# Kernel optimization log

Measured on AMD Instinct MI355X. Metric: run time of the kernel, lower is better.

Reference implementation:

```python
import jax, jax.numpy as jnp
import numpy as np

B, N, K = 4, 16384, 8
NF = [8, 32, 64, 128, 256]
E = N * K


def setup_inputs() -> dict:
    key = jax.random.key(0)
    ks = jax.random.split(key, 16)
    x = jax.random.normal(ks[0], (B, N, NF[0]), jnp.float32)
    # knn-style edge list: every node appears as a center K times (no empty segments)
    centers = jnp.tile(jnp.repeat(jnp.arange(N), K)[None, None, :], (B, 1, 1))
    neighbors = jax.random.randint(ks[1], (B, 1, E), 0, N)
    edge_index = jnp.concatenate([centers, neighbors], axis=1)
    specs = [("0a", NF[0], NF[1]), ("0b", NF[0], NF[1]),
             ("1a", NF[1], NF[2]), ("1b", NF[1], NF[2]),
             ("2a", NF[2], NF[3]), ("2b", NF[2], NF[3]),
             ("3a", NF[3], NF[4]), ("3b", NF[3], NF[4]),
             ("cat", NF[1] + NF[2] + NF[3] + NF[4], 1)]
    inp = {"x": x, "edge_index": edge_index}
    for i, (nm, ci, co) in enumerate(specs):
        inp["W" + nm] = jax.random.normal(ks[2 + i], (ci, co), jnp.float32) / np.sqrt(ci)
        inp["g" + nm] = jnp.ones((co,), jnp.float32)   # BN gamma
        inp["b" + nm] = jnp.zeros((co,), jnp.float32)  # BN beta
    inp["bias"] = jnp.zeros((1,), jnp.float32)
    return inp


def _bn(x, g, b):
    # training-mode BatchNorm1d over all rows (GraphBatchNorm1d reduces over batch*num_points)
    m = x.mean(0)
    v = jnp.mean(jnp.square(x - m), 0)  # biased variance, as torch BN uses for normalization
    return g * (x - m) * jax.lax.rsqrt(v + 1e-5) + b


def _mlp(x, W, g, b):
    # Linear(bias=False) -> BN -> LeakyReLU(0.2)
    return jax.nn.leaky_relu(_bn(x @ W, g, b), negative_slope=0.2)


def reference(x, edge_index,
              W0a, g0a, b0a, W0b, g0b, b0b,
              W1a, g1a, b1a, W1b, g1b, b1b,
              W2a, g2a, b2a, W2b, g2b, b2b,
              W3a, g3a, b3a, W3b, g3b, b3b,
              Wcat, gcat, bcat, bias):
    BN = B * N
    xf = x.reshape(BN, NF[0])
    ei = edge_index.transpose(1, 0, 2).reshape(2, -1)  # [2, B*E]
    off = jnp.repeat(jnp.arange(B) * N, E)
    centers = ei[0] + off
    neighbors = ei[1] + off
    segmax = lambda v: jax.ops.segment_max(v, centers, num_segments=BN)
    x0 = _mlp(xf, W0a, g0a, b0a) + segmax(_mlp(xf[neighbors] - xf[centers], W0b, g0b, b0b))
    x1 = _mlp(x0, W1a, g1a, b1a) + segmax(_mlp(x0, W1b, g1b, b1b)[neighbors])
    x2 = _mlp(x1, W2a, g2a, b2a) + segmax(_mlp(x1, W2b, g2b, b2b)[neighbors])
    x3 = _mlp(x2, W3a, g3a, b3a) + segmax(_mlp(x2, W3b, g3b, b3b)[neighbors])
    x_cat = _mlp(jnp.concatenate([x0, x1, x2, x3], axis=-1), Wcat, gcat, bcat)
    return x_cat + bias
```

## Files before the change

### kernel.cpp

```cpp
#include <hip/hip_runtime.h>
#include <math.h>

static constexpr int BB = 4;
static constexpr int NN = 16384;
static constexpr int KK = 8;
static constexpr int EE = 131072;
static constexpr int RR = 65536;
static constexpr int EG = 524288;

static constexpr int SPL = 64;
static constexpr size_t SLOT = (size_t)SPL*512;

static constexpr size_t OFF_X0 = 0;
static constexpr size_t OFF_X1 = OFF_X0 + (size_t)RR*32;
static constexpr size_t OFF_X2 = OFF_X1 + (size_t)RR*64;
static constexpr size_t OFF_X3 = OFF_X2 + (size_t)RR*128;
static constexpr size_t OFF_ZB = OFF_X3 + (size_t)RR*256;
static constexpr size_t OFF_ZC = OFF_ZB + (size_t)RR*128;
static constexpr size_t OFF_S  = OFF_ZC + (size_t)RR;
static constexpr size_t OFF_WP = OFF_S + 9*SLOT;
static constexpr size_t WP1_OFF = 0;
static constexpr size_t WP2_OFF = 4096;
static constexpr size_t WP3_OFF = 4096 + 16384;

__device__ __forceinline__ float lrelu(float x) { return fmaxf(x, 0.2f*x); }

__device__ __forceinline__ unsigned short f2h(float f) {
    _Float16 h = (_Float16)f;
    return *(unsigned short*)&h;
}
__device__ __forceinline__ float h2f(unsigned short u) {
    _Float16 h = *(_Float16*)&u;
    return (float)h;
}

typedef __attribute__((ext_vector_type(8))) _Float16 half8v;
typedef __attribute__((ext_vector_type(8))) unsigned short ushort8v;
typedef __attribute__((ext_vector_type(4))) float float4v;

__global__ __launch_bounds__(256) void k_l0_node(const float* __restrict__ xf,
                                                 const float* __restrict__ W,
                                                 unsigned short* __restrict__ z,
                                                 float* __restrict__ S) {
    __shared__ float w[256];
    __shared__ float red[64];
    int tid = threadIdx.x;
    w[tid] = W[tid];
    if (tid < 64) red[tid] = 0.f;
    __syncthreads();
    int r = blockIdx.x*256 + tid;
    const float4* xr = (const float4*)(xf + (size_t)r*8);
    float4 a = xr[0], b = xr[1];
    float xv[8] = {a.x,a.y,a.z,a.w,b.x,b.y,b.z,b.w};
    float op[32];
#pragma unroll
    for (int c = 0; c < 32; ++c) {
        float s = 0.f;
#pragma unroll
        for (int k = 0; k < 8; ++k) s = fmaf(xv[k], w[k*32+c], s);
        op[c] = s;
    }
    ushort8v* zp = (ushort8v*)(z + (size_t)r*32);
#pragma unroll
    for (int i = 0; i < 4; ++i) {
        ushort8v h;
#pragma unroll
        for (int j = 0; j < 8; ++j) h[j] = f2h(op[i*8+j]);
        zp[i] = h;
    }
#pragma unroll
    for (int c = 0; c < 32; ++c) {
        float s = op[c], q = op[c]*op[c];
#pragma unroll
        for (int off = 32; off >= 1; off >>= 1) {
            s += __shfl_xor(s, off, 64);
            q += __shfl_xor(q, off, 64);
        }
        if ((tid & 63) == 0) { atomicAdd(&red[c], s); atomicAdd(&red[32+c], q); }
    }
    __syncthreads();
    if (tid < 64) atomicAdd(&S[(size_t)(blockIdx.x & (SPL-1))*512 + tid], red[tid]);
}

__global__ __launch_bounds__(256) void k_edge_stats(const float* __restrict__ xf,
                                                    const int* __restrict__ ei,
                                                    const float* __restrict__ W,
                                                    float* __restrict__ S) {
    __shared__ float w[256];
    __shared__ float red[64];
    int tid = threadIdx.x;
    w[tid] = W[tid];
    if (tid < 64) red[tid] = 0.f;
    __syncthreads();
    int g = tid & 3;
    int cg = g*8;
    float s[8], q[8];
#pragma unroll
    for (int j = 0; j < 8; ++j) { s[j] = 0.f; q[j] = 0.f; }
    int qid = (blockIdx.x*256 + tid) >> 2;
    int NQ = (gridDim.x*256) >> 2;
    for (int e = qid; e < EG; e += NQ) {
        int b = e >> 17, jj = e & (EE-1);
        const int* base = ei + (size_t)b*2*EE;
        int ctr = base[jj], nbr = base[EE + jj];
        const float4* pc = (const float4*)(xf + ((size_t)(b<<14) + ctr)*8);
        const float4* pn = (const float4*)(xf + ((size_t)(b<<14) + nbr)*8);
        float4 c0 = pc[0], c1 = pc[1], n0 = pn[0], n1 = pn[1];
        float d[8] = {n0.x-c0.x, n0.y-c0.y, n0.z-c0.z, n0.w-c0.w,
                      n1.x-c1.x, n1.y-c1.y, n1.z-c1.z, n1.w-c1.w};
#pragma unroll
        for (int j = 0; j < 8; ++j) {
            int c = cg + j;
            float z = 0.f;
#pragma unroll
            for (int k = 0; k < 8; ++k) z = fmaf(d[k], w[k*32+c], z);
            s[j] += z; q[j] = fmaf(z, z, q[j]);
        }
    }
#pragma unroll
    for (int off = 4; off <= 32; off <<= 1) {
#pragma unroll
        for (int j = 0; j < 8; ++j) {
            s[j] += __shfl_xor(s[j], off, 64);
            q[j] += __shfl_xor(q[j], off, 64);
        }
    }
    if ((tid & 63) < 4) {
#pragma unroll
        for (int j = 0; j < 8; ++j) {
            atomicAdd(&red[cg + j], s[j]);
            atomicAdd(&red[32 + cg + j], q[j]);
        }
    }
    __syncthreads();
    if (tid < 64) atomicAdd(&S[(size_t)(blockIdx.x & (SPL-1))*512 + tid], red[tid]);
}

__global__ __launch_bounds__(256) void k_edge_apply(const float* __restrict__ xf,
                                                    const int* __restrict__ ei,
                                                    const float* __restrict__ W,
                                                    const float* __restrict__ Sa,
                                                    const float* __restrict__ Sb,
                                                    const float* __restrict__ ga,
                                                    const float* __restrict__ ba,
                                                    const float* __restrict__ gb,
                                                    const float* __restrict__ bbp,
                                                    const float* __restrict__ Wc,
                                                    unsigned short* __restrict__ x0,
                                                    float* __restrict__ zc) {
    __shared__ float w[256];
    __shared__ float scb[32], shb[32], sca[32], sha[32], swc[32];
    int tid = threadIdx.x;
    w[tid] = W[tid];
    if (tid < 32) {
        float su = 0.f, qu = 0.f;
        for (int p = 0; p < SPL; ++p) { su += Sa[(size_t)p*512 + tid]; qu += Sa[(size_t)p*512 + 32 + tid]; }
        float m = su*(1.f/RR);
        float v = fmaxf(qu*(1.f/RR) - m*m, 0.f);
        float sc = ga[tid]*rsqrtf(v + 1e-5f);
        sca[tid] = sc; sha[tid] = fmaf(-m, sc, ba[tid]);
        swc[tid] = Wc[tid];
    } else if (tid < 64) {
        int c = tid - 32;
        float su = 0.f, qu = 0.f;
        for (int p = 0; p < SPL; ++p) { su += Sb[(size_t)p*512 + c]; qu += Sb[(size_t)p*512 + 32 + c]; }
        float m = su*(1.f/EG);
        float v = fmaxf(qu*(1.f/EG) - m*m, 0.f);
        float sc = gb[c]*rsqrtf(v + 1e-5f);
        scb[c] = sc; shb[c] = fmaf(-m, sc, bbp[c]);
    }
    __syncthreads();
    int r = blockIdx.x*256 + tid;
    int b = r >> 14, n = r & (NN-1);
    const int* nb = ei + (size_t)b*2*EE + EE + n*KK;
    const float4* pc = (const float4*)(xf + (size_t)r*8);
    float4 c0 = pc[0], c1 = pc[1];
    float mx[32];
#pragma unroll
    for (int c = 0; c < 32; ++c) mx[c] = -3.0e38f;
    for (int k = 0; k < KK; ++k) {
        int j = nb[k];
        const float4* pn = (const float4*)(xf + ((size_t)(b<<14) + j)*8);
        float4 n0 = pn[0], n1 = pn[1];
        float d[8] = {n0.x-c0.x, n0.y-c0.y, n0.z-c0.z, n0.w-c0.w,
                      n1.x-c1.x, n1.y-c1.y, n1.z-c1.z, n1.w-c1.w};
#pragma unroll
        for (int c = 0; c < 32; ++c) {
            float z = 0.f;
#pragma unroll
            for (int k2 = 0; k2 < 8; ++k2) z = fmaf(d[k2], w[k2*32+c], z);
            float y = lrelu(fmaf(z, scb[c], shb[c]));
            mx[c] = fmaxf(mx[c], y);
        }
    }
    ushort8v* xp = (ushort8v*)(x0 + (size_t)r*32);
    float sdot = 0.f;
#pragma unroll
    for (int i = 0; i < 4; ++i) {
        ushort8v v = xp[i];
        ushort8v o;
#pragma unroll
        for (int j = 0; j < 8; ++j) {
            int c = i*8 + j;
            float val = lrelu(fmaf(h2f(v[j]), sca[c], sha[c])) + mx[c];
            o[j] = f2h(val);
            sdot = fmaf(val, swc[c], sdot);
        }
        xp[i] = o;
    }
    zc[r] = sdot;
}

template<int CI, int CO>
__global__ __launch_bounds__(256) void k_packW(const float* __restrict__ Wa,
                                               const float* __restrict__ Wb,
                                               unsigned short* __restrict__ Wp) {
    constexpr int NT = 2*CO;
    constexpr int KT = CI/32;
    int t = blockIdx.x*256 + threadIdx.x;
    if (t >= NT*CI) return;
    int ng = t % NT, k = t / NT;
    float v = (ng < CO) ? Wa[(size_t)k*CO + ng] : Wb[(size_t)k*CO + (ng - CO)];
    int nt = ng >> 4, n = ng & 15;
    int kt = k >> 5, kq = (k & 31) >> 3, j = k & 7;
    int f = nt*KT + kt;
    int idx = f*512 + ((kq*16 + n)<<3) + j;
    Wp[idx] = f2h(v);
}

template<int CI, int CO, int NCH, int MR>
__global__ __launch_bounds__(256, 4) void k_mfma_dual(const unsigned short* __restrict__ X,
                                                      const unsigned short* __restrict__ Wp,
                                                      unsigned short* __restrict__ Za,
                                                      unsigned short* __restrict__ Zb,
                                                      float* __restrict__ Sa,
                                                      float* __restrict__ Sb) {
    constexpr int KT = CI/32;
    constexpr int WCNT = NCH*KT*512;
    constexpr int ROWT = RR/(MR*16);
    constexpr int STR = NCH*16 + 8;
    constexpr int XW  = (CI < 64) ? CI : 64;
    constexpr int PLB = CO/64;
    __shared__ unsigned short Wlds[WCNT];
    __shared__ unsigned short scr[4][16*STR];
    int tid = threadIdx.x;
    int lane = tid & 63, wid = tid >> 6;
    int ch = blockIdx.y;
    int wglob = blockIdx.x*4 + wid;
    int NW = gridDim.x*4;
    int n = lane & 15, kq = lane >> 4;
    int rg = lane >> 3, c8l = (lane & 7)*8;
    unsigned short* myscr = scr[wid];
    size_t pl = (size_t)(wglob & (SPL-1)) * 512;
    bool isA = (ch < PLB);
    unsigned short* Zp = (isA ? Za : Zb) + (size_t)(isA ? ch : ch - PLB)*((size_t)RR*64);
    {
        const ushort8v* src = (const ushort8v*)(Wp + (size_t)ch*WCNT);
        ushort8v* dst = (ushort8v*)Wlds;
        for (int u = tid; u < WCNT/8; u += 256) dst[u] = src[u];
    }
    __syncthreads();

    for (int t = wglob; t < ROWT; t += NW) {
        size_t rowbase = (size_t)t * (MR*16);
        float4v acc[MR][NCH];
#pragma unroll
        for (int i = 0; i < MR; ++i)
#pragma unroll
            for (int j = 0; j < NCH; ++j)
                acc[i][j] = (float4v){0.f, 0.f, 0.f, 0.f};
#pragma unroll
        for (int kt = 0; kt < KT; ++kt) {
            int k0 = kt*32 + kq*8;
            int xpl = k0 >> 6;
            int xoff = k0 & (XW-1);
            const unsigned short* Xp = X + (size_t)xpl*((size_t)RR*64);
            half8v b[MR];
#pragma unroll
            for (int i = 0; i < MR; ++i)
                b[i] = *(const half8v*)&Xp[(rowbase + i*16 + n)*XW + xoff];
#pragma unroll
            for (int j = 0; j < NCH; ++j) {
                half8v w = *(const half8v*)&Wlds[(j*KT + kt)*512 + lane*8];
#pragma unroll
                for (int i = 0; i < MR; ++i)
                    acc[i][j] = __builtin_amdgcn_mfma_f32_16x16x32_f16(w, b[i], acc[i][j], 0, 0, 0);
            }
        }
#pragma unroll
        for (int j = 0; j < NCH; ++j) {
            int colg = ch*64 + j*16;
            float* Sg = isA ? Sa : Sb;
            int cb = isA ? colg : colg - CO;
#pragma unroll
            for (int reg = 0; reg < 4; ++reg) {
                float s = 0.f, q = 0.f;
#pragma unroll
                for (int i = 0; i < MR; ++i) {
                    float v = acc[i][j][reg];
                    s += v; q = fmaf(v, v, q);
                }
                s += __shfl_xor(s, 1, 64); q += __shfl_xor(q, 1, 64);
                s += __shfl_xor(s, 2, 64); q += __shfl_xor(q, 2, 64);
                s += __shfl_xor(s, 4, 64); q += __shfl_xor(q, 4, 64);
                s += __shfl_xor(s, 8, 64); q += __shfl_xor(q, 8, 64);
                if (n == 0) {
                    int col = cb + kq*4 + reg;
                    atomicAdd(&Sg[pl + col], s);
                    atomicAdd(&Sg[pl + CO + col], q);
                }
            }
        }
#pragma unroll
        for (int i = 0; i < MR; ++i) {
            __builtin_amdgcn_wave_barrier();
#pragma unroll
            for (int j = 0; j < NCH; ++j) {
                float4v a4 = acc[i][j];
                ushort4 h = { f2h(a4[0]), f2h(a4[1]), f2h(a4[2]), f2h(a4[3]) };
                *(ushort4*)&myscr[n*STR + j*16 + kq*4] = h;
            }
            __builtin_amdgcn_wave_barrier();
#pragma unroll
            for (int i2 = 0; i2 < 2; ++i2) {
                int rit = rg + i2*8;
                ushort8v v = *(const ushort8v*)&myscr[rit*STR + c8l];
                *(ushort8v*)&Zp[(rowbase + i*16 + rit)*64 + c8l] = v;
            }
        }
    }
}

template<int CO>
__global__ __launch_bounds__(256) void k_redstats(float* __restrict__ Sa,
                                                  float* __restrict__ Sb) {
    int t = blockIdx.x*256 + threadIdx.x;
    for (int u = t; u < 2*CO; u += gridDim.x*256) {
        float sa = 0.f, sb = 0.f;
        for (int p = 1; p < SPL; ++p) {
            sa += Sa[(size_t)p*512 + u];
            sb += Sb[(size_t)p*512 + u];
        }
        Sa[u] += sa;
        Sb[u] += sb;
    }
}

template<int CO, bool WRITEBACK>
__global__ __launch_bounds__(256) void k_gathermax(unsigned short* __restrict__ xi,
                                                   const unsigned short* __restrict__ zbh,
                                                   const int* __restrict__ ei,
                                                   const float* __restrict__ Sa,
                                                   const float* __restrict__ Sb,
                                                   const float* __restrict__ ga,
                                                   const float* __restrict__ ba,
                                                   const float* __restrict__ gb,
                                                   const float* __restrict__ bbp,
                                                   const float* __restrict__ Wc,
                                                   int wcoff,
                                                   float* __restrict__ zc) {
    constexpr int CQ = CO/8;
    __shared__ float sca[CO], sha[CO], scb[CO], shb[CO], swc[CO];
    int tid = threadIdx.x;
    for (int u = tid; u < CO; u += 256) {
        float m = Sa[u]*(1.f/RR);
        float v = fmaxf(Sa[CO+u]*(1.f/RR) - m*m, 0.f);
        float sc = ga[u]*rsqrtf(v + 1e-5f);
        sca[u] = sc; sha[u] = fmaf(-m, sc, ba[u]);
        m = Sb[u]*(1.f/RR);
        v = fmaxf(Sb[CO+u]*(1.f/RR) - m*m, 0.f);
        sc = gb[u]*rsqrtf(v + 1e-5f);
        scb[u] = sc; shb[u] = fmaf(-m, sc, bbp[u]);
        swc[u] = Wc[wcoff + u];
    }
    __syncthreads();
    int t = blockIdx.x*256 + tid;
    int r = t / CQ;
    int c8 = (t % CQ)*8;
    int pln = c8 >> 6;
    int off = c8 & 63;
    const unsigned short* zpl = zbh + (size_t)pln*((size_t)RR*64);
    unsigned short* xpl = xi + (size_t)pln*((size_t)RR*64);
    int b = r >> 14, n = r & (NN-1);
    const int* nb = ei + (size_t)b*2*EE + EE + n*KK;
    float sb[8], hb[8];
#pragma unroll
    for (int j = 0; j < 8; ++j) { sb[j] = scb[c8+j]; hb[j] = shb[c8+j]; }
    int nbr[KK];
#pragma unroll
    for (int k = 0; k < KK; ++k) nbr[k] = nb[k];
    size_t bb64 = ((size_t)(b<<14))*64 + off;
    float mx[8];
#pragma unroll
    for (int j = 0; j < 8; ++j) mx[j] = -3e38f;
#pragma unroll
    for (int k = 0; k < KK; ++k) {
        ushort8v u = *(const ushort8v*)(zpl + bb64 + (size_t)nbr[k]*64);
#pragma unroll
        for (int j = 0; j < 8; ++j)
            mx[j] = fmaxf(mx[j], lrelu(fmaf(h2f(u[j]), sb[j], hb[j])));
    }
    ushort8v* xp = (ushort8v*)&xpl[(size_t)r*64 + off];
    ushort8v a = *xp;
    float sdot = 0.f;
    if (WRITEBACK) {
        ushort8v o;
#pragma unroll
        for (int j = 0; j < 8; ++j) {
            float val = lrelu(fmaf(h2f(a[j]), sca[c8+j], sha[c8+j])) + mx[j];
            o[j] = f2h(val);
            sdot = fmaf(val, swc[c8+j], sdot);
        }
        *xp = o;
    } else {
#pragma unroll
        for (int j = 0; j < 8; ++j) {
            float val = lrelu(fmaf(h2f(a[j]), sca[c8+j], sha[c8+j])) + mx[j];
            sdot = fmaf(val, swc[c8+j], sdot);
        }
    }
#pragma unroll
    for (int w = CQ/2; w >= 1; w >>= 1) sdot += __shfl_xor(sdot, w, 64);
    int lane = tid & 63;
    if ((lane & (CQ-1)) == 0) atomicAdd(&zc[r], sdot);
}

__global__ __launch_bounds__(256) void k_catstats(const float* __restrict__ zc,
                                                  float* __restrict__ S8) {
    __shared__ float rs2[2];
    int tid = threadIdx.x;
    if (tid < 2) rs2[tid] = 0.f;
    __syncthreads();
    float v = zc[blockIdx.x*256 + tid];
    float s = v, q = v*v;
#pragma unroll
    for (int off = 32; off >= 1; off >>= 1) {
        s += __shfl_xor(s, off, 64);
        q += __shfl_xor(q, off, 64);
    }
    if ((tid & 63) == 0) { atomicAdd(&rs2[0], s); atomicAdd(&rs2[1], q); }
    __syncthreads();
    if (tid == 0) {
        int p = blockIdx.x & 255;
        atomicAdd(&S8[p*2],     rs2[0]);
        atomicAdd(&S8[p*2 + 1], rs2[1]);
    }
}

__global__ __launch_bounds__(256) void k_catfinal(const float* __restrict__ zc,
                                                  const float* __restrict__ S8,
                                                  const float* __restrict__ g,
                                                  const float* __restrict__ bb,
                                                  const float* __restrict__ bias,
                                                  float* __restrict__ out) {
    __shared__ float rs[256], rq[256];
    int tid = threadIdx.x;
    rs[tid] = S8[tid*2];
    rq[tid] = S8[tid*2 + 1];
    __syncthreads();
#pragma unroll
    for (int h = 128; h >= 1; h >>= 1) {
        if (tid < h) { rs[tid] += rs[tid+h]; rq[tid] += rq[tid+h]; }
        __syncthreads();
    }
    int r = blockIdx.x*256 + tid;
    const float invR = 1.f/65536.f;
    float m = rs[0]*invR;
    float v = fmaxf(rq[0]*invR - m*m, 0.f);
    float sc = g[0]*rsqrtf(v + 1e-5f);
    float sh = fmaf(-m, sc, bb[0]);
    float y = lrelu(fmaf(zc[r], sc, sh));
    out[r] = y + bias[0];
}

extern "C" void kernel_launch(void* const* d_in, const int* in_sizes, int n_in,
                              void* d_out, int out_size, void* d_ws, size_t ws_size,
                              hipStream_t stream) {
    const float* x    = (const float*)d_in[0];
    const int*   ei   = (const int*)d_in[1];
    const float* W0a  = (const float*)d_in[2];
    const float* g0a  = (const float*)d_in[3];
    const float* b0a  = (const float*)d_in[4];
    const float* W0b  = (const float*)d_in[5];
    const float* g0b  = (const float*)d_in[6];
    const float* b0b  = (const float*)d_in[7];
    const float* W1a  = (const float*)d_in[8];
    const float* g1a  = (const float*)d_in[9];
    const float* b1a  = (const float*)d_in[10];
    const float* W1b  = (const float*)d_in[11];
    const float* g1b  = (const float*)d_in[12];
    const float* b1b  = (const float*)d_in[13];
    const float* W2a  = (const float*)d_in[14];
    const float* g2a  = (const float*)d_in[15];
    const float* b2a  = (const float*)d_in[16];
    const float* W2b  = (const float*)d_in[17];
    const float* g2b  = (const float*)d_in[18];
    const float* b2b  = (const float*)d_in[19];
    const float* W3a  = (const float*)d_in[20];
    const float* g3a  = (const float*)d_in[21];
    const float* b3a  = (const float*)d_in[22];
    const float* W3b  = (const float*)d_in[23];
    const float* g3b  = (const float*)d_in[24];
    const float* b3b  = (const float*)d_in[25];
    const float* Wcat = (const float*)d_in[26];
    const float* gcat = (const float*)d_in[27];
    const float* bcat = (const float*)d_in[28];
    const float* bias = (const float*)d_in[29];
    float* out = (float*)d_out;

    float* ws = (float*)d_ws;
    unsigned short* x0 = (unsigned short*)(ws + OFF_X0);
    unsigned short* x1 = (unsigned short*)(ws + OFF_X1);
    unsigned short* x2 = (unsigned short*)(ws + OFF_X2);
    unsigned short* x3 = (unsigned short*)(ws + OFF_X3);
    unsigned short* zbh = (unsigned short*)(ws + OFF_ZB);
    float* zc = ws + OFF_ZC;
    float* S  = ws + OFF_S;
    unsigned short* wpbase = (unsigned short*)(ws + OFF_WP);
    unsigned short* wp1 = wpbase + WP1_OFF;
    unsigned short* wp2 = wpbase + WP2_OFF;
    unsigned short* wp3 = wpbase + WP3_OFF;
    auto Sl = [&](int i) { return S + (size_t)i*SLOT; };

    hipMemsetAsync(S, 0, 9*SLOT*sizeof(float), stream);

    k_packW<32,64><<<(128*32+255)/256, 256, 0, stream>>>(W1a, W1b, wp1);
    k_packW<64,128><<<(256*64+255)/256, 256, 0, stream>>>(W2a, W2b, wp2);
    k_packW<128,256><<<(512*128+255)/256, 256, 0, stream>>>(W3a, W3b, wp3);

    k_l0_node<<<RR/256, 256, 0, stream>>>(x, W0a, x0, Sl(0));
    k_edge_stats<<<512, 256, 0, stream>>>(x, ei, W0b, Sl(1));
    k_edge_apply<<<RR/256, 256, 0, stream>>>(x, ei, W0b, Sl(0), Sl(1),
                                             g0a, b0a, g0b, b0b, Wcat, x0, zc);

    k_mfma_dual<32,64,4,4><<<dim3(256,2), 256, 0, stream>>>(x0, wp1, x1, zbh, Sl(2), Sl(3));
    k_redstats<64><<<4, 256, 0, stream>>>(Sl(2), Sl(3));
    k_gathermax<64,true><<<RR*8/256, 256, 0, stream>>>(x1, zbh, ei, Sl(2), Sl(3),
                                                       g1a, b1a, g1b, b1b, Wcat, 32, zc);

    k_mfma_dual<64,128,4,4><<<dim3(256,4), 256, 0, stream>>>(x1, wp2, x2, zbh, Sl(4), Sl(5));
    k_redstats<128><<<4, 256, 0, stream>>>(Sl(4), Sl(5));
    k_gathermax<128,true><<<RR*16/256, 256, 0, stream>>>(x2, zbh, ei, Sl(4), Sl(5),
                                                         g2a, b2a, g2b, b2b, Wcat, 96, zc);

    k_mfma_dual<128,256,4,4><<<dim3(256,8), 256, 0, stream>>>(x2, wp3, x3, zbh, Sl(6), Sl(7));
    k_redstats<256><<<4, 256, 0, stream>>>(Sl(6), Sl(7));
    k_gathermax<256,false><<<RR*32/256, 256, 0, stream>>>(x3, zbh, ei, Sl(6), Sl(7),
                                                          g3a, b3a, g3b, b3b, Wcat, 224, zc);

    k_catstats<<<RR/256, 256, 0, stream>>>(zc, Sl(8));
    k_catfinal<<<RR/256, 256, 0, stream>>>(zc, Sl(8), gcat, bcat, bias, out);
}
```

Baseline: 316.8 us.

## Restructure dual MFMA GEMM to read weights from global and map chunks per wave

Replaces the persistent-grid dual GEMM with a kernel where each block owns a 64- or 128-row tile and each wave handles one or more 64-column weight chunks. Weights are read directly from global memory (relying on cache) instead of being staged into LDS, and output is written straight from MFMA accumulators without the LDS scratch transpose. This removes the LDS weight load, the block barrier and the LDS staging. In exchange it gives up explicit weight reuse and coalesced 16-byte output stores, and the X rows are reloaded once per chunk.

```diff
diff --git a/kernel.cpp b/kernel.cpp
--- a/kernel.cpp
+++ b/kernel.cpp
@@ -228,46 +228,39 @@
     Wp[idx] = f2h(v);
 }
 
-template<int CI, int CO, int NCH, int MR>
-__global__ __launch_bounds__(256, 4) void k_mfma_dual(const unsigned short* __restrict__ X,
-                                                      const unsigned short* __restrict__ Wp,
-                                                      unsigned short* __restrict__ Za,
-                                                      unsigned short* __restrict__ Zb,
-                                                      float* __restrict__ Sa,
-                                                      float* __restrict__ Sb) {
+template<int CI, int CO>
+__global__ __launch_bounds__(256, 4) void k_mfma_dual2(const unsigned short* __restrict__ X,
+                                                       const unsigned short* __restrict__ Wp,
+                                                       unsigned short* __restrict__ Za,
+                                                       unsigned short* __restrict__ Zb,
+                                                       float* __restrict__ Sa,
+                                                       float* __restrict__ Sb) {
     constexpr int KT = CI/32;
-    constexpr int WCNT = NCH*KT*512;
-    constexpr int ROWT = RR/(MR*16);
-    constexpr int STR = NCH*16 + 8;
+    constexpr int WCNT = 4*KT*512;
+    constexpr int NCHUNK = CO/32;
+    constexpr int PLB = CO/64;
     constexpr int XW  = (CI < 64) ? CI : 64;
-    constexpr int PLB = CO/64;
-    __shared__ unsigned short Wlds[WCNT];
-    __shared__ unsigned short scr[4][16*STR];
+    constexpr int CPW = (NCHUNK + 3)/4;
+    constexpr int RG  = (NCHUNK >= 4) ? 1 : (4/NCHUNK);
     int tid = threadIdx.x;
     int lane = tid & 63, wid = tid >> 6;
-    int ch = blockIdx.y;
-    int wglob = blockIdx.x*4 + wid;
-    int NW = gridDim.x*4;
     int n = lane & 15, kq = lane >> 4;
-    int rg = lane >> 3, c8l = (lane & 7)*8;
-    unsigned short* myscr = scr[wid];
-    size_t pl = (size_t)(wglob & (SPL-1)) * 512;
-    bool isA = (ch < PLB);
-    unsigned short* Zp = (isA ? Za : Zb) + (size_t)(isA ? ch : ch - PLB)*((size_t)RR*64);
-    {
-        const ushort8v* src = (const ushort8v*)(Wp + (size_t)ch*WCNT);
-        ushort8v* dst = (ushort8v*)Wlds;
-        for (int u = tid; u < WCNT/8; u += 256) dst[u] = src[u];
-    }
-    __syncthreads();
-
-    for (int t = wglob; t < ROWT; t += NW) {
-        size_t rowbase = (size_t)t * (MR*16);
-        float4v acc[MR][NCH];
-#pragma unroll
-        for (int i = 0; i < MR; ++i)
-#pragma unroll
-            for (int j = 0; j < NCH; ++j)
+    int rgi = (RG == 1) ? 0 : (wid >> 1);
+    int ch0 = (RG == 1) ? wid : (wid & 1);
+    size_t rowbase = ((size_t)blockIdx.x*RG + rgi)*64;
+    size_t pl = (size_t)((blockIdx.x*4 + wid) & (SPL-1))*512;
+
+#pragma unroll
+    for (int cc = 0; cc < CPW; ++cc) {
+        int ch = ch0 + cc*4;
+        bool isA = (ch < PLB);
+        unsigned short* Zp = (isA ? Za : Zb) + (size_t)(isA ? ch : ch - PLB)*((size_t)RR*64);
+        const unsigned short* Wc = Wp + (size_t)ch*WCNT;
+        float4v acc[4][4];
+#pragma unroll
+        for (int i = 0; i < 4; ++i)
+#pragma unroll
+            for (int j = 0; j < 4; ++j)
                 acc[i][j] = (float4v){0.f, 0.f, 0.f, 0.f};
 #pragma unroll
         for (int kt = 0; kt < KT; ++kt) {
@@ -275,57 +268,50 @@
             int xpl = k0 >> 6;
             int xoff = k0 & (XW-1);
             const unsigned short* Xp = X + (size_t)xpl*((size_t)RR*64);
-            half8v b[MR];
-#pragma unroll
-            for (int i = 0; i < MR; ++i)
+            half8v b[4];
+#pragma unroll
+            for (int i = 0; i < 4; ++i)
                 b[i] = *(const half8v*)&Xp[(rowbase + i*16 + n)*XW + xoff];
 #pragma unroll
-            for (int j = 0; j < NCH; ++j) {
-                half8v w = *(const half8v*)&Wlds[(j*KT + kt)*512 + lane*8];
-#pragma unroll
-                for (int i = 0; i < MR; ++i)
+            for (int j = 0; j < 4; ++j) {
+                half8v w = *(const half8v*)&Wc[(j*KT + kt)*512 + lane*8];
+#pragma unroll
+                for (int i = 0; i < 4; ++i)
                     acc[i][j] = __builtin_amdgcn_mfma_f32_16x16x32_f16(w, b[i], acc[i][j], 0, 0, 0);
             }
         }
-#pragma unroll
-        for (int j = 0; j < NCH; ++j) {
-            int colg = ch*64 + j*16;
+        {
             float* Sg = isA ? Sa : Sb;
-            int cb = isA ? colg : colg - CO;
-#pragma unroll
-            for (int reg = 0; reg < 4; ++reg) {
-                float s = 0.f, q = 0.f;
-#pragma unroll
-                for (int i = 0; i < MR; ++i) {
-                    float v = acc[i][j][reg];
-                    s += v; q = fmaf(v, v, q);
-                }
-                s += __shfl_xor(s, 1, 64); q += __shfl_xor(q, 1, 64);
-                s += __shfl_xor(s, 2, 64); q += __shfl_xor(q, 2, 64);
-                s += __shfl_xor(s, 4, 64); q += __shfl_xor(q, 4, 64);
-                s += __shfl_xor(s, 8, 64); q += __shfl_xor(q, 8, 64);
-                if (n == 0) {
-                    int col = cb + kq*4 + reg;
-                    atomicAdd(&Sg[pl + col], s);
-                    atomicAdd(&Sg[pl + CO + col], q);
+            int cb0 = isA ? ch*64 : ch*64 - CO;
+#pragma unroll
+            for (int j = 0; j < 4; ++j) {
+#pragma unroll
+                for (int reg = 0; reg < 4; ++reg) {
+                    float s = 0.f, q = 0.f;
+#pragma unroll
+                    for (int i = 0; i < 4; ++i) {
+                        float v = acc[i][j][reg];
+                        s += v; q = fmaf(v, v, q);
+                    }
+                    s += __shfl_xor(s, 1, 64); q += __shfl_xor(q, 1, 64);
+                    s += __shfl_xor(s, 2, 64); q += __shfl_xor(q, 2, 64);
+                    s += __shfl_xor(s, 4, 64); q += __shfl_xor(q, 4, 64);
+                    s += __shfl_xor(s, 8, 64); q += __shfl_xor(q, 8, 64);
+                    if (n == 0) {
+                        int col = cb0 + j*16 + kq*4 + reg;
+                        atomicAdd(&Sg[pl + col], s);
+                        atomicAdd(&Sg[pl + CO + col], q);
+                    }
                 }
             }
         }
 #pragma unroll
-        for (int i = 0; i < MR; ++i) {
-            __builtin_amdgcn_wave_barrier();
-#pragma unroll
-            for (int j = 0; j < NCH; ++j) {
+        for (int i = 0; i < 4; ++i) {
+#pragma unroll
+            for (int j = 0; j < 4; ++j) {
                 float4v a4 = acc[i][j];
                 ushort4 h = { f2h(a4[0]), f2h(a4[1]), f2h(a4[2]), f2h(a4[3]) };
-                *(ushort4*)&myscr[n*STR + j*16 + kq*4] = h;
-            }
-            __builtin_amdgcn_wave_barrier();
-#pragma unroll
-            for (int i2 = 0; i2 < 2; ++i2) {
-                int rit = rg + i2*8;
-                ushort8v v = *(const ushort8v*)&myscr[rit*STR + c8l];
-                *(ushort8v*)&Zp[(rowbase + i*16 + rit)*64 + c8l] = v;
+                *(ushort4*)&Zp[(rowbase + i*16 + n)*64 + (size_t)(j*16 + kq*4)] = h;
             }
         }
     }
@@ -533,17 +519,17 @@
     k_edge_apply<<<RR/256, 256, 0, stream>>>(x, ei, W0b, Sl(0), Sl(1),
                                              g0a, b0a, g0b, b0b, Wcat, x0, zc);
 
-    k_mfma_dual<32,64,4,4><<<dim3(256,2), 256, 0, stream>>>(x0, wp1, x1, zbh, Sl(2), Sl(3));
+    k_mfma_dual2<32,64><<<RR/128, 256, 0, stream>>>(x0, wp1, x1, zbh, Sl(2), Sl(3));
     k_redstats<64><<<4, 256, 0, stream>>>(Sl(2), Sl(3));
     k_gathermax<64,true><<<RR*8/256, 256, 0, stream>>>(x1, zbh, ei, Sl(2), Sl(3),
                                                        g1a, b1a, g1b, b1b, Wcat, 32, zc);
 
-    k_mfma_dual<64,128,4,4><<<dim3(256,4), 256, 0, stream>>>(x1, wp2, x2, zbh, Sl(4), Sl(5));
+    k_mfma_dual2<64,128><<<RR/64, 256, 0, stream>>>(x1, wp2, x2, zbh, Sl(4), Sl(5));
     k_redstats<128><<<4, 256, 0, stream>>>(Sl(4), Sl(5));
     k_gathermax<128,true><<<RR*16/256, 256, 0, stream>>>(x2, zbh, ei, Sl(4), Sl(5),
                                                          g2a, b2a, g2b, b2b, Wcat, 96, zc);
 
-    k_mfma_dual<128,256,4,4><<<dim3(256,8), 256, 0, stream>>>(x2, wp3, x3, zbh, Sl(6), Sl(7));
+    k_mfma_dual2<128,256><<<RR/64, 256, 0, stream>>>(x2, wp3, x3, zbh, Sl(6), Sl(7));
     k_redstats<256><<<4, 256, 0, stream>>>(Sl(6), Sl(7));
     k_gathermax<256,false><<<RR*32/256, 256, 0, stream>>>(x3, zbh, ei, Sl(6), Sl(7),
                                                           g3a, b3a, g3b, b3b, Wcat, 224, zc);
```

Result: slower. 342.4 us (+8.1%).

## Double-buffer X loads and defer BN stat atomics in MFMA dual GEMM

Applied to the files above, without the earlier changes.

Rewrites the dual-GEMM MFMA kernel so the X fragments for the next k-step, or the next row tile, are prefetched into a second register buffer while the current MFMAs run. Per-column sum and sum-of-squares are kept in registers across all row tiles, so the shuffle reduction and atomics happen once per wave instead of once per tile. Launch bounds change to 3 waves per SIMD and the grid is reduced for layers 2 and 3 so each wave handles more tiles. The cost is higher register pressure and fewer resident waves, and fewer blocks may leave some CUs underused.

```diff
diff --git a/kernel.cpp b/kernel.cpp
--- a/kernel.cpp
+++ b/kernel.cpp
@@ -228,16 +228,17 @@
     Wp[idx] = f2h(v);
 }
 
-template<int CI, int CO, int NCH, int MR>
-__global__ __launch_bounds__(256, 4) void k_mfma_dual(const unsigned short* __restrict__ X,
-                                                      const unsigned short* __restrict__ Wp,
-                                                      unsigned short* __restrict__ Za,
-                                                      unsigned short* __restrict__ Zb,
-                                                      float* __restrict__ Sa,
-                                                      float* __restrict__ Sb) {
+template<int CI, int CO>
+__global__ __launch_bounds__(256, 3) void k_mfma_dual3(const unsigned short* __restrict__ X,
+                                                       const unsigned short* __restrict__ Wp,
+                                                       unsigned short* __restrict__ Za,
+                                                       unsigned short* __restrict__ Zb,
+                                                       float* __restrict__ Sa,
+                                                       float* __restrict__ Sb) {
+    constexpr int NCH = 4;
     constexpr int KT = CI/32;
     constexpr int WCNT = NCH*KT*512;
-    constexpr int ROWT = RR/(MR*16);
+    constexpr int ROWT = RR/64;
     constexpr int STR = NCH*16 + 8;
     constexpr int XW  = (CI < 64) ? CI : 64;
     constexpr int PLB = CO/64;
@@ -261,58 +262,34 @@
     }
     __syncthreads();
 
-    for (int t = wglob; t < ROWT; t += NW) {
-        size_t rowbase = (size_t)t * (MR*16);
-        float4v acc[MR][NCH];
-#pragma unroll
-        for (int i = 0; i < MR; ++i)
-#pragma unroll
-            for (int j = 0; j < NCH; ++j)
-                acc[i][j] = (float4v){0.f, 0.f, 0.f, 0.f};
-#pragma unroll
-        for (int kt = 0; kt < KT; ++kt) {
-            int k0 = kt*32 + kq*8;
-            int xpl = k0 >> 6;
-            int xoff = k0 & (XW-1);
-            const unsigned short* Xp = X + (size_t)xpl*((size_t)RR*64);
-            half8v b[MR];
-#pragma unroll
-            for (int i = 0; i < MR; ++i)
-                b[i] = *(const half8v*)&Xp[(rowbase + i*16 + n)*XW + xoff];
-#pragma unroll
-            for (int j = 0; j < NCH; ++j) {
-                half8v w = *(const half8v*)&Wlds[(j*KT + kt)*512 + lane*8];
-#pragma unroll
-                for (int i = 0; i < MR; ++i)
-                    acc[i][j] = __builtin_amdgcn_mfma_f32_16x16x32_f16(w, b[i], acc[i][j], 0, 0, 0);
-            }
-        }
-#pragma unroll
-        for (int j = 0; j < NCH; ++j) {
-            int colg = ch*64 + j*16;
-            float* Sg = isA ? Sa : Sb;
-            int cb = isA ? colg : colg - CO;
-#pragma unroll
-            for (int reg = 0; reg < 4; ++reg) {
-                float s = 0.f, q = 0.f;
-#pragma unroll
-                for (int i = 0; i < MR; ++i) {
-                    float v = acc[i][j][reg];
-                    s += v; q = fmaf(v, v, q);
-                }
-                s += __shfl_xor(s, 1, 64); q += __shfl_xor(q, 1, 64);
-                s += __shfl_xor(s, 2, 64); q += __shfl_xor(q, 2, 64);
-                s += __shfl_xor(s, 4, 64); q += __shfl_xor(q, 4, 64);
-                s += __shfl_xor(s, 8, 64); q += __shfl_xor(q, 8, 64);
-                if (n == 0) {
-                    int col = cb + kq*4 + reg;
-                    atomicAdd(&Sg[pl + col], s);
-                    atomicAdd(&Sg[pl + CO + col], q);
+    float4v ps[NCH], pq[NCH];
+#pragma unroll
+    for (int j = 0; j < NCH; ++j) { ps[j] = (float4v){0,0,0,0}; pq[j] = (float4v){0,0,0,0}; }
+
+    auto issue = [&](half8v (&dst)[4], size_t rowb, int kt) {
+        int k0 = kt*32 + kq*8;
+        int xpl = k0 >> 6;
+        int xoff = k0 & (XW-1);
+        const unsigned short* Xp = X + (size_t)xpl*((size_t)RR*64);
+#pragma unroll
+        for (int i = 0; i < 4; ++i)
+            dst[i] = *(const half8v*)&Xp[(rowb + i*16 + n)*XW + xoff];
+    };
+
+    auto epilogue = [&](float4v (&acc)[4][NCH], size_t rowbase) {
+#pragma unroll
+        for (int j = 0; j < NCH; ++j)
+#pragma unroll
+            for (int i = 0; i < 4; ++i) {
+                float4v a4 = acc[i][j];
+#pragma unroll
+                for (int reg = 0; reg < 4; ++reg) {
+                    ps[j][reg] += a4[reg];
+                    pq[j][reg] = fmaf(a4[reg], a4[reg], pq[j][reg]);
                 }
             }
-        }
-#pragma unroll
-        for (int i = 0; i < MR; ++i) {
+#pragma unroll
+        for (int i = 0; i < 4; ++i) {
             __builtin_amdgcn_wave_barrier();
 #pragma unroll
             for (int j = 0; j < NCH; ++j) {
@@ -326,6 +303,80 @@
                 int rit = rg + i2*8;
                 ushort8v v = *(const ushort8v*)&myscr[rit*STR + c8l];
                 *(ushort8v*)&Zp[(rowbase + i*16 + rit)*64 + c8l] = v;
+            }
+        }
+    };
+
+    if constexpr (KT == 1) {
+        for (int t = wglob; t < ROWT; t += NW) {
+            size_t rowbase = (size_t)t*64;
+            float4v acc[4][NCH];
+#pragma unroll
+            for (int i = 0; i < 4; ++i)
+#pragma unroll
+                for (int j = 0; j < NCH; ++j) acc[i][j] = (float4v){0,0,0,0};
+            half8v b[4];
+            issue(b, rowbase, 0);
+#pragma unroll
+            for (int j = 0; j < NCH; ++j) {
+                half8v w = *(const half8v*)&Wlds[j*512 + lane*8];
+#pragma unroll
+                for (int i = 0; i < 4; ++i)
+                    acc[i][j] = __builtin_amdgcn_mfma_f32_16x16x32_f16(w, b[i], acc[i][j], 0, 0, 0);
+            }
+            epilogue(acc, rowbase);
+        }
+    } else {
+        half8v b0[4], b1[4];
+        int t = wglob;
+        if (t < ROWT) issue(b0, (size_t)t*64, 0);
+        for (; t < ROWT; t += NW) {
+            size_t rowbase = (size_t)t*64;
+            int t2 = t + NW;
+            size_t nextrb = (t2 < ROWT) ? (size_t)t2*64 : rowbase;
+            float4v acc[4][NCH];
+#pragma unroll
+            for (int i = 0; i < 4; ++i)
+#pragma unroll
+                for (int j = 0; j < NCH; ++j) acc[i][j] = (float4v){0,0,0,0};
+
+            auto step = [&](half8v (&bc)[4], half8v (&bn)[4], int kt) {
+                if (kt + 1 < KT) issue(bn, rowbase, kt + 1);
+                else             issue(bn, nextrb, 0);
+#pragma unroll
+                for (int j = 0; j < NCH; ++j) {
+                    half8v w = *(const half8v*)&Wlds[(j*KT + kt)*512 + lane*8];
+#pragma unroll
+                    for (int i = 0; i < 4; ++i)
+                        acc[i][j] = __builtin_amdgcn_mfma_f32_16x16x32_f16(w, bc[i], acc[i][j], 0, 0, 0);
+                }
+            };
+#pragma unroll
+            for (int kh = 0; kh < KT/2; ++kh) {
+                step(b0, b1, 2*kh);
+                step(b1, b0, 2*kh + 1);
+            }
+            epilogue(acc, rowbase);
+        }
+    }
+
+    {
+        float* Sg = isA ? Sa : Sb;
+        int cb0 = isA ? ch*64 : ch*64 - CO;
+#pragma unroll
+        for (int j = 0; j < NCH; ++j) {
+#pragma unroll
+            for (int reg = 0; reg < 4; ++reg) {
+                float s = ps[j][reg], q = pq[j][reg];
+                s += __shfl_xor(s, 1, 64); q += __shfl_xor(q, 1, 64);
+                s += __shfl_xor(s, 2, 64); q += __shfl_xor(q, 2, 64);
+                s += __shfl_xor(s, 4, 64); q += __shfl_xor(q, 4, 64);
+                s += __shfl_xor(s, 8, 64); q += __shfl_xor(q, 8, 64);
+                if (n == 0) {
+                    int col = cb0 + j*16 + kq*4 + reg;
+                    atomicAdd(&Sg[pl + col], s);
+                    atomicAdd(&Sg[pl + CO + col], q);
+                }
             }
         }
     }
@@ -533,17 +584,17 @@
     k_edge_apply<<<RR/256, 256, 0, stream>>>(x, ei, W0b, Sl(0), Sl(1),
                                              g0a, b0a, g0b, b0b, Wcat, x0, zc);
 
-    k_mfma_dual<32,64,4,4><<<dim3(256,2), 256, 0, stream>>>(x0, wp1, x1, zbh, Sl(2), Sl(3));
+    k_mfma_dual3<32,64><<<dim3(256,2), 256, 0, stream>>>(x0, wp1, x1, zbh, Sl(2), Sl(3));
     k_redstats<64><<<4, 256, 0, stream>>>(Sl(2), Sl(3));
     k_gathermax<64,true><<<RR*8/256, 256, 0, stream>>>(x1, zbh, ei, Sl(2), Sl(3),
                                                        g1a, b1a, g1b, b1b, Wcat, 32, zc);
 
-    k_mfma_dual<64,128,4,4><<<dim3(256,4), 256, 0, stream>>>(x1, wp2, x2, zbh, Sl(4), Sl(5));
+    k_mfma_dual3<64,128><<<dim3(192,4), 256, 0, stream>>>(x1, wp2, x2, zbh, Sl(4), Sl(5));
     k_redstats<128><<<4, 256, 0, stream>>>(Sl(4), Sl(5));
     k_gathermax<128,true><<<RR*16/256, 256, 0, stream>>>(x2, zbh, ei, Sl(4), Sl(5),
                                                          g2a, b2a, g2b, b2b, Wcat, 96, zc);
 
-    k_mfma_dual<128,256,4,4><<<dim3(256,8), 256, 0, stream>>>(x2, wp3, x3, zbh, Sl(6), Sl(7));
+    k_mfma_dual3<128,256><<<dim3(96,8), 256, 0, stream>>>(x2, wp3, x3, zbh, Sl(6), Sl(7));
     k_redstats<256><<<4, 256, 0, stream>>>(Sl(6), Sl(7));
     k_gathermax<256,false><<<RR*32/256, 256, 0, stream>>>(x3, zbh, ei, Sl(6), Sl(7),
                                                           g3a, b3a, g3b, b3b, Wcat, 224, zc);
```

New measurement: 310.7 us. No clear change (-1.9%).
